# Kernel tuning notes

Measured on AMD Instinct MI355X. Metric: run time of the kernel, lower is better.

## Reference

```python
import jax, jax.numpy as jnp
import numpy as np

CHANNELS = [(3, 64), (64, 64), (64, 128), (128, 128), (128, 256), (256, 256), (256, 256),
            (256, 512), (512, 512), (512, 512), (512, 512), (512, 512), (512, 512)]
HW = 256
IN_FEAT = 512 * (HW // 32) * (HW // 32)  # 32768


def _conv(x, w):
    # 3x3, stride 1, pad 1, NCHW / OIHW, no bias
    return jax.lax.conv_general_dilated(x, w, (1, 1), ((1, 1), (1, 1)),
                                         dimension_numbers=("NCHW", "OIHW", "NCHW"))


def _maxpool2(x):
    return jax.lax.reduce_window(x, -jnp.inf, jax.lax.max, (1, 1, 2, 2), (1, 1, 2, 2), "VALID")


def setup_inputs() -> dict:
    key = jax.random.key(0)
    keys = jax.random.split(key, 17)
    inp = {"x": jax.random.normal(keys[0], (1, 3, HW, HW), jnp.float32),
           "H": HW, "W": HW, "nTh": 32, "nTw": 32}
    for i, (cin, cout) in enumerate(CHANNELS):
        scale = (1.0 / np.sqrt(9.0 * cin)).astype(np.float32) if hasattr(np.sqrt(9.0 * cin), 'astype') else 1.0 / np.sqrt(9.0 * cin)
        inp[f"cw{i + 1}"] = jax.random.normal(keys[1 + i], (cout, cin, 3, 3), jnp.float32) * np.float32(1.0 / np.sqrt(9.0 * cin))
    inp["fw1"] = jax.random.normal(keys[14], (4096, IN_FEAT), jnp.float32) * np.float32(1.0 / np.sqrt(IN_FEAT))
    inp["fw2"] = jax.random.normal(keys[15], (4096, 4096), jnp.float32) * np.float32(1.0 / np.sqrt(4096))
    inp["fw3"] = jax.random.normal(keys[16], (1000, 4096), jnp.float32) * np.float32(1.0 / np.sqrt(4096))
    return inp


def reference(x, H, W, nTh, nTw, cw1, cw2, cw3, cw4, cw5, cw6, cw7, cw8, cw9, cw10,
              cw11, cw12, cw13, fw1, fw2, fw3):
    # VGG-16 conv stack; tiling in the original is an execution schedule only,
    # the math equals the untiled stack. conv -> relu repeated, maxpool per block.
    conv_ws = [cw1, cw2, cw3, cw4, cw5, cw6, cw7, cw8, cw9, cw10, cw11, cw12, cw13]
    blocks = [(0, 2), (2, 4), (4, 7), (7, 10), (10, 13)]
    h = x
    for lo, hi in blocks:
        for w in conv_ws[lo:hi]:
            h = jax.nn.relu(_conv(h, w))
        h = _maxpool2(h)
    h = h.reshape(h.shape[0], -1)          # [1, 32768]
    h = h @ fw1.T                           # fc1 (no bias, no relu, as in source)
    h = h @ fw2.T                           # fc2
    h = h @ fw3.T                           # fc3 -> [1, 1000]
    return h
```

## Files before the change

kernel.cpp:

```cpp
#include <hip/hip_runtime.h>
#include <cstddef>


typedef __attribute__((ext_vector_type(8))) short short8;
typedef __attribute__((ext_vector_type(4))) float f32x4;

__device__ inline unsigned short f2bf(float f) {
    unsigned int u = __builtin_bit_cast(unsigned int, f);
    u += 0x7FFF + ((u >> 16) & 1);
    return (unsigned short)(u >> 16);
}
__device__ inline float bf2f(unsigned short h) {
    unsigned int u = ((unsigned int)h) << 16;
    return __builtin_bit_cast(float, u);
}

__device__ __forceinline__ void gl_lds16(const void* src, unsigned m0v) {
    asm volatile("s_mov_b32 m0, %1\n\t"
                 "global_load_lds_dwordx4 %0, off"
                 :: "v"(src), "s"(m0v) : "memory");
}

struct WtDesc { const float* src; unsigned dst; int cin; int cout; int blk0; };
struct WtArgs { WtDesc d[12]; };

__global__ __launch_bounds__(256)
void wt_all_k(WtArgs A, unsigned short* __restrict__ wt, unsigned short* __restrict__ guard)
{
    __shared__ unsigned short lds[4][9 * 520];
    const int tid = threadIdx.x, wv = tid >> 6, lane = tid & 63;
    if (blockIdx.x == 0 && tid < 128) guard[tid] = 0;

    int l = 0;
#pragma unroll
    for (int i = 1; i < 12; ++i) l = ((int)blockIdx.x >= A.d[i].blk0) ? i : l;
    const WtDesc D = A.d[l];
    const int co = ((int)blockIdx.x - D.blk0) * 4 + wv;
    const int n = D.cin * 9;
    const int cinP = D.cin + 8;

    const float4* src = (const float4*)(D.src + (size_t)co * n);
    for (int i = lane; i < (n >> 2); i += 64) {
        float4 v = src[i];
        unsigned short b[4] = {f2bf(v.x), f2bf(v.y), f2bf(v.z), f2bf(v.w)};
        const int f0 = i * 4;
#pragma unroll
        for (int k = 0; k < 4; ++k) {
            const int f = f0 + k, ci = f / 9, pos = f - ci * 9;
            lds[wv][pos * cinP + ci] = b[k];
        }
    }
    __syncthreads();
    unsigned short* dstb = wt + D.dst;
#pragma unroll 1
    for (int pos = 0; pos < 9; ++pos) {
        unsigned short* drow = dstb + ((size_t)pos * D.cout + co) * D.cin;
        for (int c4 = lane; c4 < (D.cin >> 2); c4 += 64) {
            ushort4 u = *(const ushort4*)&lds[wv][pos * cinP + c4 * 4];
            *(ushort4*)(drow + c4 * 4) = u;
        }
    }
}

template<int PR, int MODE>
__global__ __launch_bounds__(256)
void conv_mfma_k(const unsigned short* __restrict__ act,
                 const unsigned short* __restrict__ wt,
                 const unsigned short* __restrict__ guard,
                 void* __restrict__ outp,
                 int Cin, int Cout, int H, int W, int chunkCi)
{
    constexpr int NT = PR / 4;
    constexpr int ICELLS = (PR + 2) * 18;
    constexpr int ITIN = (ICELLS * 4 + 255) / 256;
    constexpr int VL = 9 + ITIN;
    static_assert(VL == 12 || VL == 15, "unexpected stage depth");

    __shared__ __align__(16) unsigned short wLds[2][9 * 64 * 32];
    __shared__ __align__(16) unsigned short iLds[2][ITIN * 2048];

    const int tid = threadIdx.x;
    const int lane = tid & 63, wv = tid >> 6;
    const int half = lane >> 4, l15 = lane & 15;
    const int tilesX = W >> 4;
    const int pY = blockIdx.x / tilesX, pX = blockIdx.x - pY * tilesX;
    const int y0 = pY * PR, x0 = pX * 16;
    const int cob = blockIdx.y, s = blockIdx.z;
    const int ciBeg = s * chunkCi;
    const int nCh = chunkCi >> 5;

    f32x4 acc[4][NT];
#pragma unroll
    for (int mt = 0; mt < 4; ++mt)
#pragma unroll
        for (int nt = 0; nt < NT; ++nt) acc[mt][nt] = (f32x4){0.f, 0.f, 0.f, 0.f};

    auto STAGE = [&](int buf, int ci0) {
        const unsigned wB = (unsigned)(size_t)&wLds[buf][0];
        const unsigned iB = (unsigned)(size_t)&iLds[buf][0];
#pragma unroll
        for (int it = 0; it < 9; ++it) {
            const int idx = it * 256 + tid;
            const int cell = idx >> 2, q = idx & 3;
            const int pos = cell >> 6, co = cell & 63;
            const unsigned short* src = wt +
                (size_t)(pos * Cout + (cob << 6) + co) * Cin + ci0 + q * 8;
            gl_lds16(src, __builtin_amdgcn_readfirstlane(wB + (unsigned)(it * 4096 + wv * 1024)));
        }
#pragma unroll
        for (int it = 0; it < ITIN; ++it) {
            const int idx = it * 256 + tid;
            const int cell = idx >> 2, q = idx & 3;
            const int r = cell / 18, c = cell - r * 18;
            const int y = y0 - 1 + r, x = x0 - 1 + c;
            const bool ok = (idx < ICELLS * 4) & (y >= 0) & (y < H) & (x >= 0) & (x < W);
            const unsigned short* src = ok ?
                act + (size_t)(y * W + x) * Cin + ci0 + q * 8 : guard;
            gl_lds16(src, __builtin_amdgcn_readfirstlane(iB + (unsigned)(it * 4096 + wv * 1024)));
        }
    };

    STAGE(0, ciBeg);
    for (int t = 0; t < nCh; ++t) {
        const int buf = t & 1;
        if (t + 1 < nCh) {
            STAGE(buf ^ 1, ciBeg + ((t + 1) << 5));
            if constexpr (VL == 12) asm volatile("s_waitcnt vmcnt(12)" ::: "memory");
            else                    asm volatile("s_waitcnt vmcnt(15)" ::: "memory");
        } else {
            asm volatile("s_waitcnt vmcnt(0)" ::: "memory");
        }
        __builtin_amdgcn_s_barrier();
        asm volatile("" ::: "memory");

        const unsigned short* wP = wLds[buf];
        const unsigned short* iP = iLds[buf];
#pragma unroll
        for (int ky = 0; ky < 3; ++ky)
#pragma unroll
        for (int kx = 0; kx < 3; ++kx) {
            const int pos = ky * 3 + kx;
            short8 a[4];
#pragma unroll
            for (int mt = 0; mt < 4; ++mt)
                a[mt] = *(const short8*)&wP[((pos << 6) + (mt << 4) + l15) * 32 + half * 8];
#pragma unroll
            for (int nt = 0; nt < NT; ++nt) {
                const short8 b = *(const short8*)
                    &iP[((wv * NT + nt + ky) * 18 + l15 + kx) * 32 + half * 8];
#pragma unroll
                for (int mt = 0; mt < 4; ++mt)
                    acc[mt][nt] = __builtin_amdgcn_mfma_f32_16x16x32_bf16(a[mt], b, acc[mt][nt], 0, 0, 0);
            }
        }
        asm volatile("" ::: "memory");
        __builtin_amdgcn_s_barrier();
    }

    const int xg = x0 + l15;
    if (MODE == 3) {
        const int Wo = W >> 1;
#pragma unroll
        for (int mt = 0; mt < 4; ++mt)
#pragma unroll
        for (int nt = 0; nt < NT; nt += 2) {
            f32x4 a;
#pragma unroll
            for (int j = 0; j < 4; ++j) a[j] = fmaxf(acc[mt][nt][j], acc[mt][nt + 1][j]);
            f32x4 m;
#pragma unroll
            for (int j = 0; j < 4; ++j) m[j] = fmaxf(a[j], __shfl_xor(a[j], 1, 64));
            if ((l15 & 1) == 0) {
                const int yo = (y0 + wv * NT + nt) >> 1;
                const int xo = xg >> 1;
                const int co = (cob << 6) + (mt << 4) + half * 4;
                ushort4 u;
                u.x = f2bf(fmaxf(m[0], 0.f));
                u.y = f2bf(fmaxf(m[1], 0.f));
                u.z = f2bf(fmaxf(m[2], 0.f));
                u.w = f2bf(fmaxf(m[3], 0.f));
                *(ushort4*)((unsigned short*)outp + ((size_t)(yo * Wo + xo) * Cout + co)) = u;
            }
        }
    } else {
#pragma unroll
        for (int mt = 0; mt < 4; ++mt)
#pragma unroll
        for (int nt = 0; nt < NT; ++nt) {
            const int yg = y0 + wv * NT + nt;
            const int co = (cob << 6) + (mt << 4) + half * 4;
            const size_t base = (size_t)(yg * W + xg) * Cout + co;
            if (MODE == 2) {
                float4 v = make_float4(acc[mt][nt][0], acc[mt][nt][1], acc[mt][nt][2], acc[mt][nt][3]);
                *(float4*)((float*)outp + (size_t)s * Cout * H * W + base) = v;
            } else {
                ushort4 u;
                u.x = f2bf(fmaxf(acc[mt][nt][0], 0.f));
                u.y = f2bf(fmaxf(acc[mt][nt][1], 0.f));
                u.z = f2bf(fmaxf(acc[mt][nt][2], 0.f));
                u.w = f2bf(fmaxf(acc[mt][nt][3], 0.f));
                *(ushort4*)((unsigned short*)outp + base) = u;
            }
        }
    }
}

#define TILE 16
#define COB  32
__global__ __launch_bounds__(256)
void conv1_k(const float* __restrict__ in, const float* __restrict__ wt,
             unsigned short* __restrict__ out)
{
    const int Cin = 3, H = 256, W = 256, HW = H * W;
    __shared__ float sIn[2][648];
    __shared__ float sWt[2][768];

    const int tid = threadIdx.x;
    const int bx = blockIdx.x, by = blockIdx.y, co_blk = blockIdx.z;
    const int co_grp = tid >> 6;
    const int lane = tid & 63;
    const int tx = lane & 7, ty = lane >> 3;
    const int x0 = bx * TILE, y0 = by * TILE;

    int iLdsI[3], iG[3], iSub[3]; bool iOk[3];
    int wLdsI[3], wG[3], wSub[3]; bool wOk[3];
#pragma unroll
    for (int j = 0; j < 3; ++j) {
        int i = tid + j * 256;
        iOk[j] = false; iLdsI[j] = 0; iG[j] = 0; iSub[j] = 0;
        if (i < 648) {
            int sub = i / 324; int r = i - sub * 324;
            int iy = r / 18;   int ix = r - iy * 18;
            iSub[j] = sub; iLdsI[j] = sub * 324 + r;
            int y = y0 - 1 + iy, x = x0 - 1 + ix;
            if (y >= 0 && y < H && x >= 0 && x < W) { iOk[j] = true; iG[j] = sub * HW + y * W + x; }
        }
        wOk[j] = false; wLdsI[j] = 0; wG[j] = 0; wSub[j] = 0;
        if (i < 576) {
            int sub = i / 288; int r = i - sub * 288;
            int col = r / 9;   int k = r - col * 9;
            wSub[j] = sub; wLdsI[j] = sub * 384 + col * 12 + k;
            wG[j] = ((co_blk * COB + col) * Cin + sub) * 9 + k;
            wOk[j] = true;
        }
    }

    float4 acc[8];
#pragma unroll
    for (int c = 0; c < 8; ++c) acc[c] = make_float4(0.f, 0.f, 0.f, 0.f);

    const int nSteps = 2;
    float rIn[3], rWt[3];
    {
#pragma unroll
        for (int j = 0; j < 3; ++j)
            rIn[j] = (iOk[j] && iSub[j] < 3) ? in[iG[j]] : 0.f;
#pragma unroll
        for (int j = 0; j < 3; ++j)
            rWt[j] = (wOk[j] && wSub[j] < 3) ? wt[wG[j]] : 0.f;
#pragma unroll
        for (int j = 0; j < 3; ++j) { if (tid + j * 256 < 648) sIn[0][iLdsI[j]] = rIn[j]; }
#pragma unroll
        for (int j = 0; j < 3; ++j) { if (tid + j * 256 < 576) sWt[0][wLdsI[j]] = rWt[j]; }
    }

    for (int t = 0; t < nSteps; ++t) {
        __syncthreads();
        const bool more = (t + 1) < nSteps;
        if (more) {
            const int ci0 = 2;
#pragma unroll
            for (int j = 0; j < 3; ++j)
                rIn[j] = (iOk[j] && (ci0 + iSub[j]) < 3) ? in[(size_t)ci0 * HW + iG[j]] : 0.f;
#pragma unroll
            for (int j = 0; j < 3; ++j)
                rWt[j] = (wOk[j] && (ci0 + wSub[j]) < 3) ? wt[(size_t)ci0 * 9 + wG[j]] : 0.f;
        }
        const int buf = t & 1;
        const float* sI = sIn[buf];
        const float* sW = sWt[buf];
#pragma unroll
        for (int sub = 0; sub < 2; ++sub) {
            float wv[4][4];
            const float* sp = sI + sub * 324 + (2 * ty) * 18 + 2 * tx;
#pragma unroll
            for (int r = 0; r < 4; ++r) {
                float2 a = *(const float2*)(sp + r * 18);
                float2 b = *(const float2*)(sp + r * 18 + 2);
                wv[r][0] = a.x; wv[r][1] = a.y; wv[r][2] = b.x; wv[r][3] = b.y;
            }
#pragma unroll
            for (int c = 0; c < 8; ++c) {
                const float* wp = sW + sub * 384 + (co_grp * 8 + c) * 12;
                float4 w0 = *(const float4*)wp;
                float4 w1 = *(const float4*)(wp + 4);
                float  w8 = wp[8];
                const float wk[9] = {w0.x, w0.y, w0.z, w0.w, w1.x, w1.y, w1.z, w1.w, w8};
                float* ac = (float*)&acc[c];
#pragma unroll
                for (int py = 0; py < 2; ++py)
#pragma unroll
                for (int px = 0; px < 2; ++px) {
                    float sacc = ac[py * 2 + px];
#pragma unroll
                    for (int kk = 0; kk < 9; ++kk)
                        sacc = fmaf(wv[py + kk / 3][px + kk % 3], wk[kk], sacc);
                    ac[py * 2 + px] = sacc;
                }
            }
        }
        if (more) {
#pragma unroll
            for (int j = 0; j < 3; ++j) { if (tid + j * 256 < 648) sIn[buf ^ 1][iLdsI[j]] = rIn[j]; }
#pragma unroll
            for (int j = 0; j < 3; ++j) { if (tid + j * 256 < 576) sWt[buf ^ 1][wLdsI[j]] = rWt[j]; }
        }
    }

    const int co0 = co_blk * COB + co_grp * 8;
#pragma unroll
    for (int py = 0; py < 2; ++py)
#pragma unroll
    for (int px = 0; px < 2; ++px) {
        const int y = y0 + 2 * ty + py, x = x0 + 2 * tx + px;
        unsigned short u8[8];
#pragma unroll
        for (int c = 0; c < 8; ++c)
            u8[c] = f2bf(fmaxf(((const float*)&acc[c])[py * 2 + px], 0.f));
        *(uint4*)(out + (size_t)(y * W + x) * 64 + co0) = *(uint4*)u8;
    }
}

__global__ __launch_bounds__(256)
void reduce_cvt_k(const float* __restrict__ P, unsigned short* __restrict__ out,
                  int n4, int S)
{
    int i = blockIdx.x * 256 + threadIdx.x;
    if (i >= n4) return;
    const float4* p4 = (const float4*)P;
    float4 a = p4[i];
    for (int s = 1; s < S; ++s) {
        float4 b = p4[(size_t)i + (size_t)s * n4];
        a.x += b.x; a.y += b.y; a.z += b.z; a.w += b.w;
    }
    ushort4 u;
    u.x = f2bf(fmaxf(a.x, 0.f)); u.y = f2bf(fmaxf(a.y, 0.f));
    u.z = f2bf(fmaxf(a.z, 0.f)); u.w = f2bf(fmaxf(a.w, 0.f));
    *(ushort4*)(out + (size_t)i * 4) = u;
}

__global__ __launch_bounds__(256)
void reduce_pool_cvt_k(const float* __restrict__ P, unsigned short* __restrict__ out,
                       int C, int H, int W, int S)
{
    const int C4 = C >> 2, Wo = W >> 1, Ho = H >> 1;
    const int n = Ho * Wo * C4;
    int i = blockIdx.x * 256 + threadIdx.x;
    if (i >= n) return;
    const int c4 = i % C4, p = i / C4;
    const int yo = p / Wo, xo = p - yo * Wo;
    const size_t CHW = (size_t)C * H * W;
    const size_t b = (size_t)(2 * yo * W + 2 * xo) * C + c4 * 4;
    float4 v[4] = {{0,0,0,0},{0,0,0,0},{0,0,0,0},{0,0,0,0}};
    for (int s = 0; s < S; ++s) {
        const float* ps = P + s * CHW;
        float4 t0 = *(const float4*)(ps + b);
        float4 t1 = *(const float4*)(ps + b + C);
        float4 t2 = *(const float4*)(ps + b + (size_t)W * C);
        float4 t3 = *(const float4*)(ps + b + (size_t)W * C + C);
        v[0].x += t0.x; v[0].y += t0.y; v[0].z += t0.z; v[0].w += t0.w;
        v[1].x += t1.x; v[1].y += t1.y; v[1].z += t1.z; v[1].w += t1.w;
        v[2].x += t2.x; v[2].y += t2.y; v[2].z += t2.z; v[2].w += t2.w;
        v[3].x += t3.x; v[3].y += t3.y; v[3].z += t3.z; v[3].w += t3.w;
    }
    ushort4 u;
    u.x = f2bf(fmaxf(fmaxf(fmaxf(v[0].x, v[1].x), fmaxf(v[2].x, v[3].x)), 0.f));
    u.y = f2bf(fmaxf(fmaxf(fmaxf(v[0].y, v[1].y), fmaxf(v[2].y, v[3].y)), 0.f));
    u.z = f2bf(fmaxf(fmaxf(fmaxf(v[0].z, v[1].z), fmaxf(v[2].z, v[3].z)), 0.f));
    u.w = f2bf(fmaxf(fmaxf(fmaxf(v[0].w, v[1].w), fmaxf(v[2].w, v[3].w)), 0.f));
    *(ushort4*)(out + (size_t)p * C + c4 * 4) = u;
}

__global__ __launch_bounds__(256)
void reduce_pool_f32_k(const float* __restrict__ P, float* __restrict__ out,
                       int C, int H, int W, int S)
{
    const int Wo = W >> 1, Ho = H >> 1;
    const int n = Ho * Wo * C;
    int i = blockIdx.x * 256 + threadIdx.x;
    if (i >= n) return;
    const int c = i % C, p = i / C;
    const int yo = p / Wo, xo = p - yo * Wo;
    const size_t CHW = (size_t)C * H * W;
    float v0 = 0.f, v1 = 0.f, v2 = 0.f, v3 = 0.f;
    const size_t b = (size_t)(2 * yo * W + 2 * xo) * C + c;
    for (int s = 0; s < S; ++s) {
        const float* ps = P + s * CHW;
        v0 += ps[b]; v1 += ps[b + C]; v2 += ps[b + (size_t)W * C]; v3 += ps[b + (size_t)W * C + C];
    }
    out[(size_t)c * (Ho * Wo) + p] = fmaxf(fmaxf(fmaxf(v0, v1), fmaxf(v2, v3)), 0.f);
}

__global__ __launch_bounds__(256)
void gemv_k(const float* __restrict__ Wm, const float* __restrict__ xv,
            float* __restrict__ y, int K)
{
    __shared__ float red[4];
    const int tid = threadIdx.x;
    const float4* row = (const float4*)(Wm + (size_t)blockIdx.x * K);
    const float4* x4  = (const float4*)xv;
    const int K4 = K >> 2;
    float sum = 0.f;
    for (int i = tid; i < K4; i += 256) {
        float4 a = row[i], b = x4[i];
        sum += a.x * b.x + a.y * b.y + a.z * b.z + a.w * b.w;
    }
#pragma unroll
    for (int off = 32; off > 0; off >>= 1) sum += __shfl_down(sum, off, 64);
    if ((tid & 63) == 0) red[tid >> 6] = sum;
    __syncthreads();
    if (tid == 0) y[blockIdx.x] = red[0] + red[1] + red[2] + red[3];
}

extern "C" void kernel_launch(void* const* d_in, const int* in_sizes, int n_in,
                              void* d_out, int out_size, void* d_ws, size_t ws_size,
                              hipStream_t stream)
{
    (void)in_sizes; (void)n_in; (void)out_size; (void)ws_size;
    const float* x = (const float*)d_in[0];
    const float* cw[13];
    for (int i = 0; i < 13; ++i) cw[i] = (const float*)d_in[5 + i];
    const float* fw1 = (const float*)d_in[18];
    const float* fw2 = (const float*)d_in[19];
    const float* fw3 = (const float*)d_in[20];
    float* outp = (float*)d_out;

    static const int CIN[12]  = {64, 64, 128, 128, 256, 256, 256, 512, 512, 512, 512, 512};
    static const int COUT[12] = {64, 128, 128, 256, 256, 256, 512, 512, 512, 512, 512, 512};

    char* ws = (char*)d_ws;
    size_t wOff[12]; size_t o = 0;
    for (int i = 0; i < 12; ++i) { wOff[i] = o; o += (size_t)9 * COUT[i] * CIN[i]; }
    unsigned short* WT = (unsigned short*)ws;
    unsigned short* guardp = WT + o;
    size_t ao = ((o + 128) * 2 + 255) & ~(size_t)255;
    unsigned short* bA = (unsigned short*)(ws + ao);
    unsigned short* bB = (unsigned short*)(ws + ao + 8388608);
    char* Pr = ws + ao + 2 * 8388608;
    float* Pf = (float*)Pr;
    float* fcIn = (float*)bA;
    float* F1 = (float*)bB;
    float* F2 = F1 + 4096;

    WtArgs wa; int blk = 0;
    {
        size_t oo = 0;
        for (int i = 0; i < 12; ++i) {
            wa.d[i].src = cw[i + 1];
            wa.d[i].dst = (unsigned)oo;
            wa.d[i].cin = CIN[i];
            wa.d[i].cout = COUT[i];
            wa.d[i].blk0 = blk;
            oo += (size_t)9 * COUT[i] * CIN[i];
            blk += COUT[i] / 4;
        }
    }
    wt_all_k<<<blk, 256, 0, stream>>>(wa, WT, guardp);

    conv1_k<<<dim3(16, 16, 2), 256, 0, stream>>>(x, cw[0], bA);

    conv_mfma_k<16, 3><<<dim3(256, 1, 1), 256, 0, stream>>>(bA, WT + wOff[0], guardp, bB, 64, 64, 256, 256, 64);
    conv_mfma_k<8, 0><<<dim3(128, 2, 1), 256, 0, stream>>>(bB, WT + wOff[1], guardp, bA, 64, 128, 128, 128, 64);
    conv_mfma_k<8, 3><<<dim3(128, 2, 1), 256, 0, stream>>>(bA, WT + wOff[2], guardp, bB, 128, 128, 128, 128, 128);
    conv_mfma_k<8, 2><<<dim3(32, 4, 2), 256, 0, stream>>>(bB, WT + wOff[3], guardp, Pf, 128, 256, 64, 64, 64);
    reduce_cvt_k<<<(262144 + 255) / 256, 256, 0, stream>>>(Pf, bA, 262144, 2);
    conv_mfma_k<8, 2><<<dim3(32, 4, 2), 256, 0, stream>>>(bA, WT + wOff[4], guardp, Pf, 256, 256, 64, 64, 128);
    reduce_cvt_k<<<(262144 + 255) / 256, 256, 0, stream>>>(Pf, bB, 262144, 2);
    conv_mfma_k<8, 2><<<dim3(32, 4, 2), 256, 0, stream>>>(bB, WT + wOff[5], guardp, Pf, 256, 256, 64, 64, 128);
    reduce_pool_cvt_k<<<(65536 + 255) / 256, 256, 0, stream>>>(Pf, bA, 256, 64, 64, 2);
    conv_mfma_k<8, 2><<<dim3(8, 8, 4), 256, 0, stream>>>(bA, WT + wOff[6], guardp, Pf, 256, 512, 32, 32, 64);
    reduce_cvt_k<<<(131072 + 255) / 256, 256, 0, stream>>>(Pf, bB, 131072, 4);
    conv_mfma_k<8, 2><<<dim3(8, 8, 4), 256, 0, stream>>>(bB, WT + wOff[7], guardp, Pf, 512, 512, 32, 32, 128);
    reduce_cvt_k<<<(131072 + 255) / 256, 256, 0, stream>>>(Pf, bA, 131072, 4);
    conv_mfma_k<8, 2><<<dim3(8, 8, 4), 256, 0, stream>>>(bA, WT + wOff[8], guardp, Pf, 512, 512, 32, 32, 128);
    reduce_pool_cvt_k<<<(32768 + 255) / 256, 256, 0, stream>>>(Pf, bB, 512, 32, 32, 4);
    conv_mfma_k<8, 2><<<dim3(2, 8, 16), 256, 0, stream>>>(bB, WT + wOff[9], guardp, Pf, 512, 512, 16, 16, 32);
    reduce_cvt_k<<<(32768 + 255) / 256, 256, 0, stream>>>(Pf, bA, 32768, 16);
    conv_mfma_k<8, 2><<<dim3(2, 8, 16), 256, 0, stream>>>(bA, WT + wOff[10], guardp, Pf, 512, 512, 16, 16, 32);
    reduce_cvt_k<<<(32768 + 255) / 256, 256, 0, stream>>>(Pf, bB, 32768, 16);
    conv_mfma_k<8, 2><<<dim3(2, 8, 16), 256, 0, stream>>>(bB, WT + wOff[11], guardp, Pf, 512, 512, 16, 16, 32);
    reduce_pool_f32_k<<<(32768 + 255) / 256, 256, 0, stream>>>(Pf, fcIn, 512, 16, 16, 16);

    gemv_k<<<4096, 256, 0, stream>>>(fw1, fcIn, F1, 32768);
    gemv_k<<<4096, 256, 0, stream>>>(fw2, F1, F2, 4096);
    gemv_k<<<1000, 256, 0, stream>>>(fw3, F2, outp, 4096);
}
```

Baseline: 972.6 us.

## Fuse conv 2-13 and reductions into one persistent kernel with grid barriers

```diff
diff --git a/kernel.cpp b/kernel.cpp
--- a/kernel.cpp
+++ b/kernel.cpp
@@ -62,13 +62,29 @@
     }
 }
 
+__device__ __forceinline__ void gridbar(unsigned* cnt, unsigned& gen)
+{
+    __syncthreads();
+    if (threadIdx.x == 0) {
+        gen += 256;
+        __threadfence();
+        __hip_atomic_fetch_add(cnt, 1u, __ATOMIC_RELAXED, __HIP_MEMORY_SCOPE_AGENT);
+        while (__hip_atomic_load(cnt, __ATOMIC_RELAXED, __HIP_MEMORY_SCOPE_AGENT) < gen)
+            __builtin_amdgcn_s_sleep(8);
+        __threadfence();
+    }
+    __syncthreads();
+}
+
 template<int PR, int MODE>
-__global__ __launch_bounds__(256)
-void conv_mfma_k(const unsigned short* __restrict__ act,
-                 const unsigned short* __restrict__ wt,
-                 const unsigned short* __restrict__ guard,
-                 void* __restrict__ outp,
-                 int Cin, int Cout, int H, int W, int chunkCi)
+__device__ __forceinline__ void conv_stage(
+    unsigned short* wLdsA, unsigned short* iLdsA,
+    const unsigned short* __restrict__ act,
+    const unsigned short* __restrict__ wt,
+    const unsigned short* __restrict__ guard,
+    void* __restrict__ outp,
+    int Cin, int Cout, int H, int W, int chunkCi,
+    int vx, int vy, int vz, int tid)
 {
     constexpr int NT = PR / 4;
     constexpr int ICELLS = (PR + 2) * 18;
@@ -76,16 +92,12 @@
     constexpr int VL = 9 + ITIN;
     static_assert(VL == 12 || VL == 15, "unexpected stage depth");
 
-    __shared__ __align__(16) unsigned short wLds[2][9 * 64 * 32];
-    __shared__ __align__(16) unsigned short iLds[2][ITIN * 2048];
-
-    const int tid = threadIdx.x;
     const int lane = tid & 63, wv = tid >> 6;
     const int half = lane >> 4, l15 = lane & 15;
     const int tilesX = W >> 4;
-    const int pY = blockIdx.x / tilesX, pX = blockIdx.x - pY * tilesX;
+    const int pY = vx / tilesX, pX = vx - pY * tilesX;
     const int y0 = pY * PR, x0 = pX * 16;
-    const int cob = blockIdx.y, s = blockIdx.z;
+    const int cob = vy, s = vz;
     const int ciBeg = s * chunkCi;
     const int nCh = chunkCi >> 5;
 
@@ -96,8 +108,8 @@
         for (int nt = 0; nt < NT; ++nt) acc[mt][nt] = (f32x4){0.f, 0.f, 0.f, 0.f};
 
     auto STAGE = [&](int buf, int ci0) {
-        const unsigned wB = (unsigned)(size_t)&wLds[buf][0];
-        const unsigned iB = (unsigned)(size_t)&iLds[buf][0];
+        const unsigned wB = (unsigned)(size_t)(wLdsA + buf * 18432);
+        const unsigned iB = (unsigned)(size_t)(iLdsA + buf * (ITIN * 2048));
 #pragma unroll
         for (int it = 0; it < 9; ++it) {
             const int idx = it * 256 + tid;
@@ -133,8 +145,8 @@
         __builtin_amdgcn_s_barrier();
         asm volatile("" ::: "memory");
 
-        const unsigned short* wP = wLds[buf];
-        const unsigned short* iP = iLds[buf];
+        const unsigned short* wP = wLdsA + buf * 18432;
+        const unsigned short* iP = iLdsA + buf * (ITIN * 2048);
 #pragma unroll
         for (int ky = 0; ky < 3; ++ky)
 #pragma unroll
@@ -205,6 +217,153 @@
     }
 }
 
+__device__ __forceinline__ void st_reduce_cvt(const float* __restrict__ P,
+                                              unsigned short* __restrict__ out,
+                                              int n4, int S, int bid, int tid)
+{
+    const float4* p4 = (const float4*)P;
+    for (int i = bid * 256 + tid; i < n4; i += 65536) {
+        float4 a = p4[i];
+        for (int s = 1; s < S; ++s) {
+            float4 b = p4[(size_t)i + (size_t)s * n4];
+            a.x += b.x; a.y += b.y; a.z += b.z; a.w += b.w;
+        }
+        ushort4 u;
+        u.x = f2bf(fmaxf(a.x, 0.f)); u.y = f2bf(fmaxf(a.y, 0.f));
+        u.z = f2bf(fmaxf(a.z, 0.f)); u.w = f2bf(fmaxf(a.w, 0.f));
+        *(ushort4*)(out + (size_t)i * 4) = u;
+    }
+}
+
+__device__ __forceinline__ void st_reduce_pool_cvt(const float* __restrict__ P,
+                                                   unsigned short* __restrict__ out,
+                                                   int C, int H, int W, int S,
+                                                   int bid, int tid)
+{
+    const int C4 = C >> 2, Wo = W >> 1, Ho = H >> 1;
+    const int n = Ho * Wo * C4;
+    const size_t CHW = (size_t)C * H * W;
+    for (int i = bid * 256 + tid; i < n; i += 65536) {
+        const int c4 = i % C4, p = i / C4;
+        const int yo = p / Wo, xo = p - yo * Wo;
+        const size_t b = (size_t)(2 * yo * W + 2 * xo) * C + c4 * 4;
+        float4 v[4] = {{0,0,0,0},{0,0,0,0},{0,0,0,0},{0,0,0,0}};
+        for (int s = 0; s < S; ++s) {
+            const float* ps = P + s * CHW;
+            float4 t0 = *(const float4*)(ps + b);
+            float4 t1 = *(const float4*)(ps + b + C);
+            float4 t2 = *(const float4*)(ps + b + (size_t)W * C);
+            float4 t3 = *(const float4*)(ps + b + (size_t)W * C + C);
+            v[0].x += t0.x; v[0].y += t0.y; v[0].z += t0.z; v[0].w += t0.w;
+            v[1].x += t1.x; v[1].y += t1.y; v[1].z += t1.z; v[1].w += t1.w;
+            v[2].x += t2.x; v[2].y += t2.y; v[2].z += t2.z; v[2].w += t2.w;
+            v[3].x += t3.x; v[3].y += t3.y; v[3].z += t3.z; v[3].w += t3.w;
+        }
+        ushort4 u;
+        u.x = f2bf(fmaxf(fmaxf(fmaxf(v[0].x, v[1].x), fmaxf(v[2].x, v[3].x)), 0.f));
+        u.y = f2bf(fmaxf(fmaxf(fmaxf(v[0].y, v[1].y), fmaxf(v[2].y, v[3].y)), 0.f));
+        u.z = f2bf(fmaxf(fmaxf(fmaxf(v[0].z, v[1].z), fmaxf(v[2].z, v[3].z)), 0.f));
+        u.w = f2bf(fmaxf(fmaxf(fmaxf(v[0].w, v[1].w), fmaxf(v[2].w, v[3].w)), 0.f));
+        *(ushort4*)(out + (size_t)p * C + c4 * 4) = u;
+    }
+}
+
+__device__ __forceinline__ void st_reduce_pool_f32(const float* __restrict__ P,
+                                                   float* __restrict__ out,
+                                                   int C, int H, int W, int S,
+                                                   int bid, int tid)
+{
+    const int Wo = W >> 1, Ho = H >> 1;
+    const int n = Ho * Wo * C;
+    const size_t CHW = (size_t)C * H * W;
+    for (int i = bid * 256 + tid; i < n; i += 65536) {
+        const int c = i % C, p = i / C;
+        const int yo = p / Wo, xo = p - yo * Wo;
+        float v0 = 0.f, v1 = 0.f, v2 = 0.f, v3 = 0.f;
+        const size_t b = (size_t)(2 * yo * W + 2 * xo) * C + c;
+        for (int s = 0; s < S; ++s) {
+            const float* ps = P + s * CHW;
+            v0 += ps[b]; v1 += ps[b + C]; v2 += ps[b + (size_t)W * C]; v3 += ps[b + (size_t)W * C + C];
+        }
+        out[(size_t)c * (Ho * Wo) + p] = fmaxf(fmaxf(fmaxf(v0, v1), fmaxf(v2, v3)), 0.f);
+    }
+}
+
+struct MegaArgs {
+    const unsigned short* WT;
+    const unsigned short* guard;
+    unsigned short* bA;
+    unsigned short* bB;
+    float* Pf;
+    float* fcIn;
+    unsigned* cnt;
+    unsigned wOff[12];
+};
+
+__global__ __launch_bounds__(256, 1)
+void mega_k(MegaArgs A)
+{
+    __shared__ __align__(16) unsigned short wLds[2 * 18432];
+    __shared__ __align__(16) unsigned short iLds[2 * 6 * 2048];
+    const int bid = blockIdx.x, tid = threadIdx.x;
+    unsigned gen = 0;
+    unsigned* cnt = A.cnt;
+
+    conv_stage<16, 3>(wLds, iLds, A.bA, A.WT + A.wOff[0], A.guard, A.bB,
+                      64, 64, 256, 256, 64, bid, 0, 0, tid);
+    gridbar(cnt, gen);
+    conv_stage<8, 0>(wLds, iLds, A.bB, A.WT + A.wOff[1], A.guard, A.bA,
+                     64, 128, 128, 128, 64, bid & 127, bid >> 7, 0, tid);
+    gridbar(cnt, gen);
+    conv_stage<8, 3>(wLds, iLds, A.bA, A.WT + A.wOff[2], A.guard, A.bB,
+                     128, 128, 128, 128, 128, bid & 127, bid >> 7, 0, tid);
+    gridbar(cnt, gen);
+    conv_stage<8, 2>(wLds, iLds, A.bB, A.WT + A.wOff[3], A.guard, A.Pf,
+                     128, 256, 64, 64, 64, bid & 31, (bid >> 5) & 3, bid >> 7, tid);
+    gridbar(cnt, gen);
+    st_reduce_cvt(A.Pf, A.bA, 262144, 2, bid, tid);
+    gridbar(cnt, gen);
+    conv_stage<8, 2>(wLds, iLds, A.bA, A.WT + A.wOff[4], A.guard, A.Pf,
+                     256, 256, 64, 64, 128, bid & 31, (bid >> 5) & 3, bid >> 7, tid);
+    gridbar(cnt, gen);
+    st_reduce_cvt(A.Pf, A.bB, 262144, 2, bid, tid);
+    gridbar(cnt, gen);
+    conv_stage<8, 2>(wLds, iLds, A.bB, A.WT + A.wOff[5], A.guard, A.Pf,
+                     256, 256, 64, 64, 128, bid & 31, (bid >> 5) & 3, bid >> 7, tid);
+    gridbar(cnt, gen);
+    st_reduce_pool_cvt(A.Pf, A.bA, 256, 64, 64, 2, bid, tid);
+    gridbar(cnt, gen);
+    conv_stage<8, 2>(wLds, iLds, A.bA, A.WT + A.wOff[6], A.guard, A.Pf,
+                     256, 512, 32, 32, 64, bid & 7, (bid >> 3) & 7, bid >> 6, tid);
+    gridbar(cnt, gen);
+    st_reduce_cvt(A.Pf, A.bB, 131072, 4, bid, tid);
+    gridbar(cnt, gen);
+    conv_stage<8, 2>(wLds, iLds, A.bB, A.WT + A.wOff[7], A.guard, A.Pf,
+                     512, 512, 32, 32, 128, bid & 7, (bid >> 3) & 7, bid >> 6, tid);
+    gridbar(cnt, gen);
+    st_reduce_cvt(A.Pf, A.bA, 131072, 4, bid, tid);
+    gridbar(cnt, gen);
+    conv_stage<8, 2>(wLds, iLds, A.bA, A.WT + A.wOff[8], A.guard, A.Pf,
+                     512, 512, 32, 32, 128, bid & 7, (bid >> 3) & 7, bid >> 6, tid);
+    gridbar(cnt, gen);
+    st_reduce_pool_cvt(A.Pf, A.bB, 512, 32, 32, 4, bid, tid);
+    gridbar(cnt, gen);
+    conv_stage<8, 2>(wLds, iLds, A.bB, A.WT + A.wOff[9], A.guard, A.Pf,
+                     512, 512, 16, 16, 32, bid & 1, (bid >> 1) & 7, bid >> 4, tid);
+    gridbar(cnt, gen);
+    st_reduce_cvt(A.Pf, A.bA, 32768, 16, bid, tid);
+    gridbar(cnt, gen);
+    conv_stage<8, 2>(wLds, iLds, A.bA, A.WT + A.wOff[10], A.guard, A.Pf,
+                     512, 512, 16, 16, 32, bid & 1, (bid >> 1) & 7, bid >> 4, tid);
+    gridbar(cnt, gen);
+    st_reduce_cvt(A.Pf, A.bB, 32768, 16, bid, tid);
+    gridbar(cnt, gen);
+    conv_stage<8, 2>(wLds, iLds, A.bB, A.WT + A.wOff[11], A.guard, A.Pf,
+                     512, 512, 16, 16, 32, bid & 1, (bid >> 1) & 7, bid >> 4, tid);
+    gridbar(cnt, gen);
+    st_reduce_pool_f32(A.Pf, A.fcIn, 512, 16, 16, 16, bid, tid);
+}
+
 #define TILE 16
 #define COB  32
 __global__ __launch_bounds__(256)
@@ -329,76 +488,6 @@
             u8[c] = f2bf(fmaxf(((const float*)&acc[c])[py * 2 + px], 0.f));
         *(uint4*)(out + (size_t)(y * W + x) * 64 + co0) = *(uint4*)u8;
     }
-}
-
-__global__ __launch_bounds__(256)
-void reduce_cvt_k(const float* __restrict__ P, unsigned short* __restrict__ out,
-                  int n4, int S)
-{
-    int i = blockIdx.x * 256 + threadIdx.x;
-    if (i >= n4) return;
-    const float4* p4 = (const float4*)P;
-    float4 a = p4[i];
-    for (int s = 1; s < S; ++s) {
-        float4 b = p4[(size_t)i + (size_t)s * n4];
-        a.x += b.x; a.y += b.y; a.z += b.z; a.w += b.w;
-    }
-    ushort4 u;
-    u.x = f2bf(fmaxf(a.x, 0.f)); u.y = f2bf(fmaxf(a.y, 0.f));
-    u.z = f2bf(fmaxf(a.z, 0.f)); u.w = f2bf(fmaxf(a.w, 0.f));
-    *(ushort4*)(out + (size_t)i * 4) = u;
-}
-
-__global__ __launch_bounds__(256)
-void reduce_pool_cvt_k(const float* __restrict__ P, unsigned short* __restrict__ out,
-                       int C, int H, int W, int S)
-{
-    const int C4 = C >> 2, Wo = W >> 1, Ho = H >> 1;
-    const int n = Ho * Wo * C4;
-    int i = blockIdx.x * 256 + threadIdx.x;
-    if (i >= n) return;
-    const int c4 = i % C4, p = i / C4;
-    const int yo = p / Wo, xo = p - yo * Wo;
-    const size_t CHW = (size_t)C * H * W;
-    const size_t b = (size_t)(2 * yo * W + 2 * xo) * C + c4 * 4;
-    float4 v[4] = {{0,0,0,0},{0,0,0,0},{0,0,0,0},{0,0,0,0}};
-    for (int s = 0; s < S; ++s) {
-        const float* ps = P + s * CHW;
-        float4 t0 = *(const float4*)(ps + b);
-        float4 t1 = *(const float4*)(ps + b + C);
-        float4 t2 = *(const float4*)(ps + b + (size_t)W * C);
-        float4 t3 = *(const float4*)(ps + b + (size_t)W * C + C);
-        v[0].x += t0.x; v[0].y += t0.y; v[0].z += t0.z; v[0].w += t0.w;
-        v[1].x += t1.x; v[1].y += t1.y; v[1].z += t1.z; v[1].w += t1.w;
-        v[2].x += t2.x; v[2].y += t2.y; v[2].z += t2.z; v[2].w += t2.w;
-        v[3].x += t3.x; v[3].y += t3.y; v[3].z += t3.z; v[3].w += t3.w;
-    }
-    ushort4 u;
-    u.x = f2bf(fmaxf(fmaxf(fmaxf(v[0].x, v[1].x), fmaxf(v[2].x, v[3].x)), 0.f));
-    u.y = f2bf(fmaxf(fmaxf(fmaxf(v[0].y, v[1].y), fmaxf(v[2].y, v[3].y)), 0.f));
-    u.z = f2bf(fmaxf(fmaxf(fmaxf(v[0].z, v[1].z), fmaxf(v[2].z, v[3].z)), 0.f));
-    u.w = f2bf(fmaxf(fmaxf(fmaxf(v[0].w, v[1].w), fmaxf(v[2].w, v[3].w)), 0.f));
-    *(ushort4*)(out + (size_t)p * C + c4 * 4) = u;
-}
-
-__global__ __launch_bounds__(256)
-void reduce_pool_f32_k(const float* __restrict__ P, float* __restrict__ out,
-                       int C, int H, int W, int S)
-{
-    const int Wo = W >> 1, Ho = H >> 1;
-    const int n = Ho * Wo * C;
-    int i = blockIdx.x * 256 + threadIdx.x;
-    if (i >= n) return;
-    const int c = i % C, p = i / C;
-    const int yo = p / Wo, xo = p - yo * Wo;
-    const size_t CHW = (size_t)C * H * W;
-    float v0 = 0.f, v1 = 0.f, v2 = 0.f, v3 = 0.f;
-    const size_t b = (size_t)(2 * yo * W + 2 * xo) * C + c;
-    for (int s = 0; s < S; ++s) {
-        const float* ps = P + s * CHW;
-        v0 += ps[b]; v1 += ps[b + C]; v2 += ps[b + (size_t)W * C]; v3 += ps[b + (size_t)W * C + C];
-    }
-    out[(size_t)c * (Ho * Wo) + p] = fmaxf(fmaxf(fmaxf(v0, v1), fmaxf(v2, v3)), 0.f);
 }
 
 __global__ __launch_bounds__(256)
@@ -448,9 +537,12 @@
     unsigned short* bB = (unsigned short*)(ws + ao + 8388608);
     char* Pr = ws + ao + 2 * 8388608;
     float* Pf = (float*)Pr;
+    unsigned* cnt = (unsigned*)(Pr + 8388608);
     float* fcIn = (float*)bA;
     float* F1 = (float*)bB;
     float* F2 = F1 + 4096;
+
+    hipMemsetAsync(cnt, 0, 256, stream);
 
     WtArgs wa; int blk = 0;
     {
@@ -469,27 +561,11 @@
 
     conv1_k<<<dim3(16, 16, 2), 256, 0, stream>>>(x, cw[0], bA);
 
-    conv_mfma_k<16, 3><<<dim3(256, 1, 1), 256, 0, stream>>>(bA, WT + wOff[0], guardp, bB, 64, 64, 256, 256, 64);
-    conv_mfma_k<8, 0><<<dim3(128, 2, 1), 256, 0, stream>>>(bB, WT + wOff[1], guardp, bA, 64, 128, 128, 128, 64);
-    conv_mfma_k<8, 3><<<dim3(128, 2, 1), 256, 0, stream>>>(bA, WT + wOff[2], guardp, bB, 128, 128, 128, 128, 128);
-    conv_mfma_k<8, 2><<<dim3(32, 4, 2), 256, 0, stream>>>(bB, WT + wOff[3], guardp, Pf, 128, 256, 64, 64, 64);
-    reduce_cvt_k<<<(262144 + 255) / 256, 256, 0, stream>>>(Pf, bA, 262144, 2);
-    conv_mfma_k<8, 2><<<dim3(32, 4, 2), 256, 0, stream>>>(bA, WT + wOff[4], guardp, Pf, 256, 256, 64, 64, 128);
-    reduce_cvt_k<<<(262144 + 255) / 256, 256, 0, stream>>>(Pf, bB, 262144, 2);
-    conv_mfma_k<8, 2><<<dim3(32, 4, 2), 256, 0, stream>>>(bB, WT + wOff[5], guardp, Pf, 256, 256, 64, 64, 128);
-    reduce_pool_cvt_k<<<(65536 + 255) / 256, 256, 0, stream>>>(Pf, bA, 256, 64, 64, 2);
-    conv_mfma_k<8, 2><<<dim3(8, 8, 4), 256, 0, stream>>>(bA, WT + wOff[6], guardp, Pf, 256, 512, 32, 32, 64);
-    reduce_cvt_k<<<(131072 + 255) / 256, 256, 0, stream>>>(Pf, bB, 131072, 4);
-    conv_mfma_k<8, 2><<<dim3(8, 8, 4), 256, 0, stream>>>(bB, WT + wOff[7], guardp, Pf, 512, 512, 32, 32, 128);
-    reduce_cvt_k<<<(131072 + 255) / 256, 256, 0, stream>>>(Pf, bA, 131072, 4);
-    conv_mfma_k<8, 2><<<dim3(8, 8, 4), 256, 0, stream>>>(bA, WT + wOff[8], guardp, Pf, 512, 512, 32, 32, 128);
-    reduce_pool_cvt_k<<<(32768 + 255) / 256, 256, 0, stream>>>(Pf, bB, 512, 32, 32, 4);
-    conv_mfma_k<8, 2><<<dim3(2, 8, 16), 256, 0, stream>>>(bB, WT + wOff[9], guardp, Pf, 512, 512, 16, 16, 32);
-    reduce_cvt_k<<<(32768 + 255) / 256, 256, 0, stream>>>(Pf, bA, 32768, 16);
-    conv_mfma_k<8, 2><<<dim3(2, 8, 16), 256, 0, stream>>>(bA, WT + wOff[10], guardp, Pf, 512, 512, 16, 16, 32);
-    reduce_cvt_k<<<(32768 + 255) / 256, 256, 0, stream>>>(Pf, bB, 32768, 16);
-    conv_mfma_k<8, 2><<<dim3(2, 8, 16), 256, 0, stream>>>(bB, WT + wOff[11], guardp, Pf, 512, 512, 16, 16, 32);
-    reduce_pool_f32_k<<<(32768 + 255) / 256, 256, 0, stream>>>(Pf, fcIn, 512, 16, 16, 16);
+    MegaArgs ma;
+    ma.WT = WT; ma.guard = guardp; ma.bA = bA; ma.bB = bB;
+    ma.Pf = Pf; ma.fcIn = fcIn; ma.cnt = cnt;
+    for (int i = 0; i < 12; ++i) ma.wOff[i] = (unsigned)wOff[i];
+    mega_k<<<256, 256, 0, stream>>>(ma);
 
     gemv_k<<<4096, 256, 0, stream>>>(fw1, fcIn, F1, 32768);
     gemv_k<<<4096, 256, 0, stream>>>(fw2, F1, F2, 4096);
```

Measured after the change: 1.368 ms. +40.7%, slower.
